# Performance work log

Measured on AMD Instinct MI355X. Metric: run time of the kernel, lower is better.

The kernel has to match this reference:

```python
import jax, jax.numpy as jnp
import numpy as np

HID = 128; L = 4; N = 100000; E = 1600000; B = 512; OUT = 1
NVOC = 101; EVOC = 21

def layer_norm(x, g, b, eps=1e-5):
    m = x.mean(-1, keepdims=True)
    v = ((x - m) ** 2).mean(-1, keepdims=True)
    return (x - m) * jax.lax.rsqrt(v + eps) * g + b

def setup_inputs() -> dict:
    key = jax.random.key(0)
    ks = jax.random.split(key, 20)
    s = 1.0 / np.sqrt(HID)
    return {
        "x_idx": jax.random.randint(ks[0], (N,), 0, NVOC),
        "edge_index": jax.random.randint(ks[1], (2, E), 0, N),
        "edge_attr": jax.random.randint(ks[2], (E, 3), 0, EVOC),
        "batch": jnp.sort(jax.random.randint(ks[3], (N,), 0, B)),
        "node_emb": jax.random.normal(ks[4], (NVOC, HID), jnp.float32) * 0.02,
        "e1": jax.random.normal(ks[5], (EVOC, HID), jnp.float32) * 0.02,
        "e2": jax.random.normal(ks[6], (EVOC, HID), jnp.float32) * 0.02,
        "e3": jax.random.normal(ks[7], (EVOC, HID), jnp.float32) * 0.02,
        "W1": jax.random.normal(ks[8], (L, HID, HID), jnp.float32) * s,
        "b1": jnp.zeros((L, HID), jnp.float32),
        "W2": jax.random.normal(ks[9], (L, HID, HID), jnp.float32) * s,
        "b2": jnp.zeros((L, HID), jnp.float32),
        "ln_g": jnp.ones((L, HID), jnp.float32),
        "ln_b": jnp.zeros((L, HID), jnp.float32),
        "pW1": jax.random.normal(ks[10], (HID, HID), jnp.float32) * s,
        "pb1": jnp.zeros((HID,), jnp.float32),
        "pW2": jax.random.normal(ks[11], (HID, HID), jnp.float32) * s,
        "pb2": jnp.zeros((HID,), jnp.float32),
        "pg": jnp.ones((HID,), jnp.float32),
        "pbn": jnp.zeros((HID,), jnp.float32),
        "oW": jax.random.normal(ks[12], (HID, OUT), jnp.float32) * s,
        "ob": jnp.zeros((OUT,), jnp.float32),
    }

def reference(x_idx, edge_index, edge_attr, batch, node_emb, e1, e2, e3,
              W1, b1, W2, b2, ln_g, ln_b, pW1, pb1, pW2, pb2, pg, pbn, oW, ob):
    # input embedding (inmlp) and bond embedding (edge_emb1+2+3)
    x = node_emb[x_idx]                                   # [N, H]
    bond = e1[edge_attr[:, 0]] + e2[edge_attr[:, 1]] + e3[edge_attr[:, 2]]  # [E, H]
    src, dst = edge_index[0], edge_index[1]
    # residual GINEConv stack: x = x + nn((1+eps)*x + sum_j relu(x_j + bond))
    for l in range(L):
        msg = jax.nn.relu(x[src] + bond)                  # gather + fuse
        agg = jax.ops.segment_sum(msg, dst, num_segments=N)  # scatter-add
        h = x + agg                                       # eps = 0
        h = jax.nn.relu(h @ W1[l] + b1[l])
        h = h @ W2[l] + b2[l]
        h = jax.nn.relu(layer_norm(h, ln_g[l], ln_b[l]))
        x = x + h
    # node-level mean pool per graph (node_pool='mean')
    sums = jax.ops.segment_sum(x, batch, num_segments=B)  # [B, H]
    cnt = jax.ops.segment_sum(jnp.ones((N, 1), x.dtype), batch, num_segments=B)
    g = sums / jnp.maximum(cnt, 1.0)
    h = jax.nn.relu(g @ pW1 + pb1)
    h = h @ pW2 + pb2
    h = jax.nn.relu(layer_norm(h, pg, pbn))
    return jax.nn.sigmoid(h @ oW + ob)                    # [B, 1]
```

## Files before the change

### kernel.cpp

```cpp
#include <hip/hip_runtime.h>

#define HID 128
#define NN  100000
#define EE  1600000
#define BB  512
#define LL  4

typedef __attribute__((ext_vector_type(8))) short bf16x8;
typedef __attribute__((ext_vector_type(4))) float f32x4;

__device__ __forceinline__ unsigned short f32_to_bf16(float f) {
    union { float f; unsigned u; } c; c.f = f;
    unsigned r = c.u + 0x7FFFu + ((c.u >> 16) & 1u);
    return (unsigned short)(r >> 16);
}
__device__ __forceinline__ float bf16_to_f32(unsigned short h) {
    union { unsigned u; float f; } c; c.u = ((unsigned)h) << 16; return c.f;
}

__global__ __launch_bounds__(256) void hist_kernel(
    const int* __restrict__ ei, int* __restrict__ R)
{
    int e = blockIdx.x * 256 + threadIdx.x;
    if (e >= EE) return;
    atomicAdd(&R[ei[EE + e] + 1], 1);
}

__global__ __launch_bounds__(256) void scan1_kernel(int* __restrict__ R,
                                                    int* __restrict__ aux, int n)
{
    __shared__ int sh[256];
    int base = blockIdx.x * 1024;
    int t = threadIdx.x;
    int v[4]; int s = 0;
#pragma unroll
    for (int i = 0; i < 4; ++i) {
        int idx = base + t * 4 + i;
        v[i] = (idx < n) ? R[idx] : 0;
        s += v[i];
    }
    sh[t] = s; __syncthreads();
#pragma unroll
    for (int off = 1; off < 256; off <<= 1) {
        int val = (t >= off) ? sh[t - off] : 0;
        __syncthreads();
        sh[t] += val;
        __syncthreads();
    }
    int run = (t == 0) ? 0 : sh[t - 1];
#pragma unroll
    for (int i = 0; i < 4; ++i) {
        int idx = base + t * 4 + i;
        run += v[i];
        if (idx < n) R[idx] = run;
    }
    if (t == 255) aux[blockIdx.x] = sh[255];
}

__global__ __launch_bounds__(128) void scan2_kernel(int* __restrict__ aux, int nb)
{
    __shared__ int sh[128];
    int t = threadIdx.x;
    sh[t] = (t < nb) ? aux[t] : 0;
    __syncthreads();
#pragma unroll
    for (int off = 1; off < 128; off <<= 1) {
        int val = (t >= off) ? sh[t - off] : 0;
        __syncthreads();
        sh[t] += val;
        __syncthreads();
    }
    if (t < nb) aux[t] = sh[t];
}

__global__ __launch_bounds__(256) void scan3_kernel(int* __restrict__ R,
                                                    const int* __restrict__ aux, int n)
{
    int b = blockIdx.x + 1;
    int add = aux[b - 1];
#pragma unroll
    for (int i = 0; i < 4; ++i) {
        int idx = b * 1024 + threadIdx.x * 4 + i;
        if (idx < n) R[idx] += add;
    }
}

__global__ __launch_bounds__(256) void fill_kernel(
    const int* __restrict__ ei, const int* __restrict__ ea,
    int* __restrict__ R, unsigned int* __restrict__ csr)
{
    int e = blockIdx.x * 256 + threadIdx.x;
    if (e >= EE) return;
    int pos = atomicAdd(&R[ei[EE + e]], 1);
    unsigned int rec = (unsigned int)ei[e]
                     | ((unsigned int)ea[e * 3 + 0] << 17)
                     | ((unsigned int)ea[e * 3 + 1] << 22)
                     | ((unsigned int)ea[e * 3 + 2] << 27);
    csr[pos] = rec;
}

__global__ __launch_bounds__(256) void embed_kernel(
    const int* __restrict__ x_idx, const float* __restrict__ node_emb,
    float* __restrict__ x)
{
    int t = blockIdx.x * 256 + threadIdx.x;
    int node = t >> 5, j = t & 31;
    if (node >= NN) return;
    ((float4*)x)[node * 32 + j] =
        ((const float4*)node_emb)[x_idx[node] * 32 + j];
}

__device__ __forceinline__ float4 edge_term(
    unsigned int rec, int l32, const float* __restrict__ x,
    const float* __restrict__ e1, const float* __restrict__ e2,
    const float* __restrict__ e3)
{
    int src = rec & 0x1FFFF;
    int i0 = (rec >> 17) & 31, i1 = (rec >> 22) & 31, i2 = (rec >> 27) & 31;
    float4 v  = ((const float4*)x )[src * 32 + l32];
    float4 w1 = ((const float4*)e1)[i0  * 32 + l32];
    float4 w2 = ((const float4*)e2)[i1  * 32 + l32];
    float4 w3 = ((const float4*)e3)[i2  * 32 + l32];
    float4 r;
    r.x = fmaxf(v.x + w1.x + w2.x + w3.x, 0.f);
    r.y = fmaxf(v.y + w1.y + w2.y + w3.y, 0.f);
    r.z = fmaxf(v.z + w1.z + w2.z + w3.z, 0.f);
    r.w = fmaxf(v.w + w1.w + w2.w + w3.w, 0.f);
    return r;
}

__global__ __launch_bounds__(256, 8) void gather_kernel(
    const float* __restrict__ x,
    const float* __restrict__ e1, const float* __restrict__ e2,
    const float* __restrict__ e3,
    const int* __restrict__ rowend, const unsigned int* __restrict__ csr,
    float* __restrict__ agg)
{
    int wid  = (blockIdx.x * 256 + threadIdx.x) >> 6;
    int lane = threadIdx.x & 63;
    int half = lane >> 5;
    int l32  = lane & 31;
    if (wid >= NN) return;
    int beg = (wid == 0) ? 0 : rowend[wid - 1];
    int end = rowend[wid];

    float4 a0 = make_float4(0.f, 0.f, 0.f, 0.f);
    float4 a1 = make_float4(0.f, 0.f, 0.f, 0.f);
    float4 a2 = make_float4(0.f, 0.f, 0.f, 0.f);
    float4 a3 = make_float4(0.f, 0.f, 0.f, 0.f);
    int p = beg + half;
    for (; p + 6 < end; p += 8) {
        unsigned int r0 = csr[p];
        unsigned int r1 = csr[p + 2];
        unsigned int r2 = csr[p + 4];
        unsigned int r3 = csr[p + 6];
        float4 t0 = edge_term(r0, l32, x, e1, e2, e3);
        float4 t1 = edge_term(r1, l32, x, e1, e2, e3);
        float4 t2 = edge_term(r2, l32, x, e1, e2, e3);
        float4 t3 = edge_term(r3, l32, x, e1, e2, e3);
        a0.x += t0.x; a0.y += t0.y; a0.z += t0.z; a0.w += t0.w;
        a1.x += t1.x; a1.y += t1.y; a1.z += t1.z; a1.w += t1.w;
        a2.x += t2.x; a2.y += t2.y; a2.z += t2.z; a2.w += t2.w;
        a3.x += t3.x; a3.y += t3.y; a3.z += t3.z; a3.w += t3.w;
    }
    for (; p < end; p += 2) {
        float4 t0 = edge_term(csr[p], l32, x, e1, e2, e3);
        a0.x += t0.x; a0.y += t0.y; a0.z += t0.z; a0.w += t0.w;
    }
    float4 acc;
    acc.x = (a0.x + a1.x) + (a2.x + a3.x);
    acc.y = (a0.y + a1.y) + (a2.y + a3.y);
    acc.z = (a0.z + a1.z) + (a2.z + a3.z);
    acc.w = (a0.w + a1.w) + (a2.w + a3.w);
    acc.x += __shfl_xor(acc.x, 32);
    acc.y += __shfl_xor(acc.y, 32);
    acc.z += __shfl_xor(acc.z, 32);
    acc.w += __shfl_xor(acc.w, 32);
    if (half == 0)
        ((float4*)agg)[wid * 32 + l32] = acc;
}

__global__ __launch_bounds__(256) void wprep_kernel(
    const float* __restrict__ W1, const float* __restrict__ W2,
    unsigned short* __restrict__ wf)
{
    int t = blockIdx.x * 256 + threadIdx.x;
    if (t >= LL * 2 * 16384) return;
    int layer = t >> 15;
    int rem = t & 32767;
    int mat = rem >> 14;
    int idx = rem & 16383;
    int k = idx >> 7, n = idx & 127;
    const float* W = (mat ? W2 : W1) + layer * 16384;
    float w = W[k * 128 + n];
    unsigned short hi = f32_to_bf16(w);
    unsigned short lo = f32_to_bf16(w - bf16_to_f32(hi));
    int nb = n >> 4, nl = n & 15, kstep = k >> 5, quad = (k >> 3) & 3, j = k & 7;
    int di = ((nb * 4 + kstep) * 64 + (quad * 16 + nl)) * 8 + j;
    unsigned short* base = wf + (size_t)((layer * 2 + mat) * 2) * 16384;
    base[di] = hi;
    base[16384 + di] = lo;
}

__global__ __launch_bounds__(256) void edge_kernel(
    const float* __restrict__ x, const int* __restrict__ ei,
    const int* __restrict__ ea, const float* __restrict__ e1,
    const float* __restrict__ e2, const float* __restrict__ e3,
    float* __restrict__ agg)
{
    int t = blockIdx.x * 256 + threadIdx.x;
    int e = t >> 5, j = t & 31;
    if (e >= EE) return;
    int src = ei[e];
    int dst = ei[EE + e];
    int a0 = ea[e * 3 + 0], a1 = ea[e * 3 + 1], a2 = ea[e * 3 + 2];
    float4 v  = ((const float4*)x )[src * 32 + j];
    float4 w1 = ((const float4*)e1)[a0  * 32 + j];
    float4 w2 = ((const float4*)e2)[a1  * 32 + j];
    float4 w3 = ((const float4*)e3)[a2  * 32 + j];
    float mx = fmaxf(v.x + w1.x + w2.x + w3.x, 0.f);
    float my = fmaxf(v.y + w1.y + w2.y + w3.y, 0.f);
    float mz = fmaxf(v.z + w1.z + w2.z + w3.z, 0.f);
    float mw = fmaxf(v.w + w1.w + w2.w + w3.w, 0.f);
    float* ag = agg + (size_t)dst * HID + j * 4;
    atomicAdd(ag + 0, mx);
    atomicAdd(ag + 1, my);
    atomicAdd(ag + 2, mz);
    atomicAdd(ag + 3, mw);
}

#define TPAD 136
#define UPAD 132

__global__ __launch_bounds__(256) void mlp_mfma_kernel(
    const float* __restrict__ xin, const float* __restrict__ agg,
    const unsigned short* __restrict__ wf,
    const float* __restrict__ b1, const float* __restrict__ b2,
    const float* __restrict__ gamma, const float* __restrict__ beta,
    float* __restrict__ x)
{
    __shared__ __align__(16) char smemA[17408];
    __shared__ __align__(16) unsigned short t_hi[32 * TPAD];
    __shared__ __align__(16) unsigned short t_lo[32 * TPAD];
    unsigned short* h_hi = (unsigned short*)smemA;
    unsigned short* h_lo = (unsigned short*)(smemA + 8704);
    float* u_s = (float*)smemA;

    int tid = threadIdx.x;
    int rbase = blockIdx.x * 32;

    for (int idx = tid; idx < 32 * 32; idx += 256) {
        int r = idx >> 5, c4 = idx & 31;
        float4 xv = ((const float4*)xin)[(rbase + r) * 32 + c4];
        float4 av = ((const float4*)agg)[(rbase + r) * 32 + c4];
        float h0 = xv.x + av.x, h1 = xv.y + av.y;
        float h2 = xv.z + av.z, h3 = xv.w + av.w;
        unsigned short i0 = f32_to_bf16(h0), i1 = f32_to_bf16(h1);
        unsigned short i2 = f32_to_bf16(h2), i3 = f32_to_bf16(h3);
        ushort4 vh = make_ushort4(i0, i1, i2, i3);
        ushort4 vl = make_ushort4(f32_to_bf16(h0 - bf16_to_f32(i0)),
                                  f32_to_bf16(h1 - bf16_to_f32(i1)),
                                  f32_to_bf16(h2 - bf16_to_f32(i2)),
                                  f32_to_bf16(h3 - bf16_to_f32(i3)));
        int o = r * TPAD + c4 * 4;
        *(ushort4*)&h_hi[o] = vh;
        *(ushort4*)&h_lo[o] = vl;
    }
    __syncthreads();

    int lane = tid & 63;
    int wave = tid >> 6;
    int rb   = wave & 1;
    int cbg  = (wave >> 1) * 4;
    int quad = lane >> 4, nl = lane & 15;
    int arow = rb * 16 + nl;

    const unsigned short* w1_hi = wf;
    const unsigned short* w1_lo = wf + 16384;
    const unsigned short* w2_hi = wf + 32768;
    const unsigned short* w2_lo = wf + 49152;

    {
        f32x4 acc[4] = {};
#pragma unroll
        for (int ks = 0; ks < 4; ++ks) {
            int koff = ks * 32 + quad * 8;
            bf16x8 a_hi = *(const bf16x8*)&h_hi[arow * TPAD + koff];
            bf16x8 a_lo = *(const bf16x8*)&h_lo[arow * TPAD + koff];
#pragma unroll
            for (int cb = 0; cb < 4; ++cb) {
                int off = (((cbg + cb) * 4 + ks) * 64 + lane) * 8;
                bf16x8 b_hi = *(const bf16x8*)&w1_hi[off];
                bf16x8 b_lo = *(const bf16x8*)&w1_lo[off];
                acc[cb] = __builtin_amdgcn_mfma_f32_16x16x32_bf16(a_hi, b_hi, acc[cb], 0, 0, 0);
                acc[cb] = __builtin_amdgcn_mfma_f32_16x16x32_bf16(a_lo, b_hi, acc[cb], 0, 0, 0);
                acc[cb] = __builtin_amdgcn_mfma_f32_16x16x32_bf16(a_hi, b_lo, acc[cb], 0, 0, 0);
            }
        }
#pragma unroll
        for (int cb = 0; cb < 4; ++cb) {
            int col = (cbg + cb) * 16 + nl;
            float bv = b1[col];
#pragma unroll
            for (int r = 0; r < 4; ++r) {
                int row = rb * 16 + quad * 4 + r;
                float v = fmaxf(acc[cb][r] + bv, 0.f);
                unsigned short hi = f32_to_bf16(v);
                t_hi[row * TPAD + col] = hi;
                t_lo[row * TPAD + col] = f32_to_bf16(v - bf16_to_f32(hi));
            }
        }
    }
    __syncthreads();

    {
        f32x4 acc[4] = {};
#pragma unroll
        for (int ks = 0; ks < 4; ++ks) {
            int koff = ks * 32 + quad * 8;
            bf16x8 a_hi = *(const bf16x8*)&t_hi[arow * TPAD + koff];
            bf16x8 a_lo = *(const bf16x8*)&t_lo[arow * TPAD + koff];
#pragma unroll
            for (int cb = 0; cb < 4; ++cb) {
                int off = (((cbg + cb) * 4 + ks) * 64 + lane) * 8;
                bf16x8 b_hi = *(const bf16x8*)&w2_hi[off];
                bf16x8 b_lo = *(const bf16x8*)&w2_lo[off];
                acc[cb] = __builtin_amdgcn_mfma_f32_16x16x32_bf16(a_hi, b_hi, acc[cb], 0, 0, 0);
                acc[cb] = __builtin_amdgcn_mfma_f32_16x16x32_bf16(a_lo, b_hi, acc[cb], 0, 0, 0);
                acc[cb] = __builtin_amdgcn_mfma_f32_16x16x32_bf16(a_hi, b_lo, acc[cb], 0, 0, 0);
            }
        }
#pragma unroll
        for (int cb = 0; cb < 4; ++cb) {
            int col = (cbg + cb) * 16 + nl;
            float bv = b2[col];
#pragma unroll
            for (int r = 0; r < 4; ++r) {
                int row = rb * 16 + quad * 4 + r;
                u_s[row * UPAD + col] = acc[cb][r] + bv;
            }
        }
    }
    __syncthreads();

    {
        int tc = tid & 31, tr = tid >> 5;
        float4 gv  = ((const float4*)gamma)[tc];
        float4 btv = ((const float4*)beta )[tc];
#pragma unroll
        for (int j = 0; j < 4; ++j) {
            float4 u4 = *(const float4*)&u_s[(tr * 4 + j) * UPAD + tc * 4];
            float s = u4.x + u4.y + u4.z + u4.w;
            float q = u4.x*u4.x + u4.y*u4.y + u4.z*u4.z + u4.w*u4.w;
#pragma unroll
            for (int off = 1; off < 32; off <<= 1) {
                s += __shfl_xor(s, off, 64);
                q += __shfl_xor(q, off, 64);
            }
            float m   = s * (1.f / 128.f);
            float var = q * (1.f / 128.f) - m * m;
            float rs  = rsqrtf(var + 1e-5f);
            int r = rbase + tr * 4 + j;
            float4 xo = ((float4*)x)[r * 32 + tc];
            float4 o;
            o.x = xo.x + fmaxf((u4.x - m) * rs * gv.x + btv.x, 0.f);
            o.y = xo.y + fmaxf((u4.y - m) * rs * gv.y + btv.y, 0.f);
            o.z = xo.z + fmaxf((u4.z - m) * rs * gv.z + btv.z, 0.f);
            o.w = xo.w + fmaxf((u4.w - m) * rs * gv.w + btv.w, 0.f);
            ((float4*)x)[r * 32 + tc] = o;
        }
    }
}

__global__ __launch_bounds__(256) void gemm_relu_kernel(
    const float* __restrict__ x, const float* __restrict__ agg,
    const float* __restrict__ W, const float* __restrict__ bias,
    float* __restrict__ t)
{
    __shared__ float h_s[32 * 129];
    int tid = threadIdx.x;
    int tc = tid & 31, tr = tid >> 5;
    int rbase = blockIdx.x * 32;
    for (int idx = tid; idx < 32 * 128; idx += 256) {
        int r = idx >> 7, k = idx & 127;
        int g = (rbase + r) * HID + k;
        h_s[r * 129 + k] = x[g] + agg[g];
    }
    __syncthreads();
    float acc[4][4] = {};
    const float4* W4 = (const float4*)W;
#pragma unroll 4
    for (int k = 0; k < 128; ++k) {
        float4 w = W4[k * 32 + tc];
#pragma unroll
        for (int j = 0; j < 4; ++j) {
            float hv = h_s[(tr * 4 + j) * 129 + k];
            acc[j][0] = fmaf(hv, w.x, acc[j][0]);
            acc[j][1] = fmaf(hv, w.y, acc[j][1]);
            acc[j][2] = fmaf(hv, w.z, acc[j][2]);
            acc[j][3] = fmaf(hv, w.w, acc[j][3]);
        }
    }
    float4 bv = ((const float4*)bias)[tc];
#pragma unroll
    for (int j = 0; j < 4; ++j) {
        int r = rbase + tr * 4 + j;
        float4 o;
        o.x = fmaxf(acc[j][0] + bv.x, 0.f);
        o.y = fmaxf(acc[j][1] + bv.y, 0.f);
        o.z = fmaxf(acc[j][2] + bv.z, 0.f);
        o.w = fmaxf(acc[j][3] + bv.w, 0.f);
        ((float4*)t)[r * 32 + tc] = o;
    }
}

__global__ __launch_bounds__(256) void gemm_ln_res_kernel(
    const float* __restrict__ t, const float* __restrict__ W,
    const float* __restrict__ bias, const float* __restrict__ gamma,
    const float* __restrict__ beta, float* __restrict__ x)
{
    __shared__ float h_s[32 * 129];
    int tid = threadIdx.x;
    int tc = tid & 31, tr = tid >> 5;
    int rbase = blockIdx.x * 32;
    for (int idx = tid; idx < 32 * 128; idx += 256) {
        int r = idx >> 7, k = idx & 127;
        h_s[r * 129 + k] = t[(rbase + r) * HID + k];
    }
    __syncthreads();
    float acc[4][4] = {};
    const float4* W4 = (const float4*)W;
#pragma unroll 4
    for (int k = 0; k < 128; ++k) {
        float4 w = W4[k * 32 + tc];
#pragma unroll
        for (int j = 0; j < 4; ++j) {
            float hv = h_s[(tr * 4 + j) * 129 + k];
            acc[j][0] = fmaf(hv, w.x, acc[j][0]);
            acc[j][1] = fmaf(hv, w.y, acc[j][1]);
            acc[j][2] = fmaf(hv, w.z, acc[j][2]);
            acc[j][3] = fmaf(hv, w.w, acc[j][3]);
        }
    }
    float4 bv  = ((const float4*)bias )[tc];
    float4 gv  = ((const float4*)gamma)[tc];
    float4 btv = ((const float4*)beta )[tc];
#pragma unroll
    for (int j = 0; j < 4; ++j) {
        acc[j][0] += bv.x; acc[j][1] += bv.y;
        acc[j][2] += bv.z; acc[j][3] += bv.w;
        float s = acc[j][0] + acc[j][1] + acc[j][2] + acc[j][3];
        float q = acc[j][0]*acc[j][0] + acc[j][1]*acc[j][1]
                + acc[j][2]*acc[j][2] + acc[j][3]*acc[j][3];
#pragma unroll
        for (int off = 1; off < 32; off <<= 1) {
            s += __shfl_xor(s, off, 64);
            q += __shfl_xor(q, off, 64);
        }
        float m   = s * (1.f / 128.f);
        float var = q * (1.f / 128.f) - m * m;
        float rs  = rsqrtf(var + 1e-5f);
        int r = rbase + tr * 4 + j;
        float4 xo = ((float4*)x)[r * 32 + tc];
        float4 o;
        o.x = xo.x + fmaxf((acc[j][0] - m) * rs * gv.x + btv.x, 0.f);
        o.y = xo.y + fmaxf((acc[j][1] - m) * rs * gv.y + btv.y, 0.f);
        o.z = xo.z + fmaxf((acc[j][2] - m) * rs * gv.z + btv.z, 0.f);
        o.w = xo.w + fmaxf((acc[j][3] - m) * rs * gv.w + btv.w, 0.f);
        ((float4*)x)[r * 32 + tc] = o;
    }
}

#define PCHUNK 32
__global__ __launch_bounds__(256) void pool_kernel(
    const float* __restrict__ x, const int* __restrict__ batch,
    float* __restrict__ sums, int* __restrict__ cnt)
{
    int wave = (blockIdx.x * 256 + threadIdx.x) >> 6;
    int lane = threadIdx.x & 63;
    int n0 = wave * PCHUNK;
    if (n0 >= NN) return;
    int n1 = n0 + PCHUNK; if (n1 > NN) n1 = NN;

    float2 acc = make_float2(0.f, 0.f);
    int cur = batch[n0];
    int run = 0;
    for (int n = n0; n < n1; ++n) {
        int b = batch[n];
        if (b != cur) {
            float* sp = sums + cur * HID + lane * 2;
            atomicAdd(sp + 0, acc.x);
            atomicAdd(sp + 1, acc.y);
            if (lane == 0) atomicAdd(&cnt[cur], run);
            acc = make_float2(0.f, 0.f);
            run = 0; cur = b;
        }
        float2 v = ((const float2*)x)[(size_t)n * 64 + lane];
        acc.x += v.x; acc.y += v.y; ++run;
    }
    float* sp = sums + cur * HID + lane * 2;
    atomicAdd(sp + 0, acc.x);
    atomicAdd(sp + 1, acc.y);
    if (lane == 0) atomicAdd(&cnt[cur], run);
}

__global__ __launch_bounds__(128) void head_kernel(
    const float* __restrict__ sums, const int* __restrict__ cnt,
    const float* __restrict__ pW1, const float* __restrict__ pb1,
    const float* __restrict__ pW2, const float* __restrict__ pb2,
    const float* __restrict__ pg, const float* __restrict__ pbn,
    const float* __restrict__ oW, const float* __restrict__ ob,
    float* __restrict__ out)
{
    __shared__ float s0[128], s1[128], red[4];
    int b = blockIdx.x, c = threadIdx.x;

    float cn = fmaxf((float)cnt[b], 1.f);
    s0[c] = sums[b * HID + c] / cn;
    __syncthreads();

    float a = pb1[c];
#pragma unroll 4
    for (int k = 0; k < HID; ++k) a = fmaf(s0[k], pW1[k * HID + c], a);
    a = fmaxf(a, 0.f);
    s1[c] = a;
    __syncthreads();

    float u = pb2[c];
#pragma unroll 4
    for (int k = 0; k < HID; ++k) u = fmaf(s1[k], pW2[k * HID + c], u);

    float s = u, q = u * u;
#pragma unroll
    for (int off = 1; off < 64; off <<= 1) {
        s += __shfl_xor(s, off, 64);
        q += __shfl_xor(q, off, 64);
    }
    if ((c & 63) == 0) { red[(c >> 6) * 2] = s; red[(c >> 6) * 2 + 1] = q; }
    __syncthreads();
    float S = red[0] + red[2], Q = red[1] + red[3];
    float m = S * (1.f / 128.f);
    float var = Q * (1.f / 128.f) - m * m;
    float rs = rsqrtf(var + 1e-5f);
    float v = fmaxf((u - m) * rs * pg[c] + pbn[c], 0.f);

    float p = v * oW[c];
#pragma unroll
    for (int off = 1; off < 64; off <<= 1) p += __shfl_xor(p, off, 64);
    __syncthreads();
    if ((c & 63) == 0) red[c >> 6] = p;
    __syncthreads();
    if (c == 0) {
        float tot = red[0] + red[1] + ob[0];
        out[b] = 1.f / (1.f + expf(-tot));
    }
}

extern "C" void kernel_launch(void* const* d_in, const int* in_sizes, int n_in,
                              void* d_out, int out_size, void* d_ws, size_t ws_size,
                              hipStream_t stream)
{
    const int*   x_idx    = (const int*)d_in[0];
    const int*   ei       = (const int*)d_in[1];
    const int*   ea       = (const int*)d_in[2];
    const int*   batch    = (const int*)d_in[3];
    const float* node_emb = (const float*)d_in[4];
    const float* e1       = (const float*)d_in[5];
    const float* e2       = (const float*)d_in[6];
    const float* e3       = (const float*)d_in[7];
    const float* W1       = (const float*)d_in[8];
    const float* b1       = (const float*)d_in[9];
    const float* W2       = (const float*)d_in[10];
    const float* b2       = (const float*)d_in[11];
    const float* lg       = (const float*)d_in[12];
    const float* lb       = (const float*)d_in[13];
    const float* pW1      = (const float*)d_in[14];
    const float* pb1      = (const float*)d_in[15];
    const float* pW2      = (const float*)d_in[16];
    const float* pb2      = (const float*)d_in[17];
    const float* pg       = (const float*)d_in[18];
    const float* pbn      = (const float*)d_in[19];
    const float* oW       = (const float*)d_in[20];
    const float* ob       = (const float*)d_in[21];
    float* out = (float*)d_out;

    char* base = (char*)d_ws;
    size_t Sx = (size_t)NN * HID * sizeof(float);
    float* x    = (float*)(base);
    float* agg  = (float*)(base + Sx);
    float* sums = (float*)(base + 2 * Sx);
    int*   cnt  = (int*)  (base + 2 * Sx + BB * HID * 4);
    int*   R    = (int*)  (base + 2 * Sx + BB * HID * 4 + 2048);
    unsigned int* csr = (unsigned int*)((char*)R + 400016);
    int*   aux  = (int*)  ((char*)csr + (size_t)EE * 4);
    unsigned short* wf = (unsigned short*)((char*)aux + 512);
    size_t need = ((char*)wf + (size_t)LL * 2 * 2 * 16384 * 2) - base;

    bool fast = (ws_size >= need);

    embed_kernel<<<(NN * 32 + 255) / 256, 256, 0, stream>>>(x_idx, node_emb, x);

    if (fast) {
        const int n = NN + 1, NB = (n + 1023) / 1024;
        hipMemsetAsync(R, 0, (size_t)n * sizeof(int), stream);
        hist_kernel <<<(EE + 255) / 256, 256, 0, stream>>>(ei, R);
        scan1_kernel<<<NB, 256, 0, stream>>>(R, aux, n);
        scan2_kernel<<<1, 128, 0, stream>>>(aux, NB);
        scan3_kernel<<<NB - 1, 256, 0, stream>>>(R, aux, n);
        fill_kernel <<<(EE + 255) / 256, 256, 0, stream>>>(ei, ea, R, csr);
        wprep_kernel<<<(LL * 2 * 16384 + 255) / 256, 256, 0, stream>>>(W1, W2, wf);
    }

    for (int l = 0; l < LL; ++l) {
        if (fast) {
            gather_kernel<<<(NN * 64 + 255) / 256, 256, 0, stream>>>(
                x, e1, e2, e3, R, csr, agg);
            mlp_mfma_kernel<<<NN / 32, 256, 0, stream>>>(
                x, agg, wf + (size_t)l * 65536,
                b1 + l * HID, b2 + l * HID,
                lg + l * HID, lb + l * HID, x);
        } else {
            hipMemsetAsync(agg, 0, Sx, stream);
            edge_kernel<<<(EE * 32 + 255) / 256, 256, 0, stream>>>(
                x, ei, ea, e1, e2, e3, agg);
            gemm_relu_kernel<<<NN / 32, 256, 0, stream>>>(
                x, agg, W1 + l * HID * HID, b1 + l * HID, agg);
            gemm_ln_res_kernel<<<NN / 32, 256, 0, stream>>>(
                agg, W2 + l * HID * HID, b2 + l * HID,
                lg + l * HID, lb + l * HID, x);
        }
    }

    hipMemsetAsync(sums, 0,
                   (size_t)BB * HID * sizeof(float) + BB * sizeof(int), stream);
    {
        int waves = (NN + PCHUNK - 1) / PCHUNK;
        int blocks = (waves + 3) / 4;
        pool_kernel<<<blocks, 256, 0, stream>>>(x, batch, sums, cnt);
    }
    head_kernel<<<BB, 128, 0, stream>>>(
        sums, cnt, pW1, pb1, pW2, pb2, pg, pbn, oW, ob, out);
}
```

Measured before the change: 1.326 ms.

## Fuse CSR gather with MLP into one per-layer kernel using ping-pong x buffers

Merges the per-node CSR gather and the two-GEMM MLP with LayerNorm into a single kernel per layer. Each block handles 16 nodes, and each wave gathers 4 nodes straight into bf16 hi/lo shared tiles. The agg buffer is replaced by double-buffered x to avoid read/write hazards across blocks. This removes the write and re-read of the 51 MB agg tensor and one launch per layer. In exchange, MFMA tiles shrink to 16 rows, so weight reuse per block is lower, and gather latency is no longer overlapped with GEMM work inside the block.

```diff
diff --git a/kernel.cpp b/kernel.cpp
--- a/kernel.cpp
+++ b/kernel.cpp
@@ -5,6 +5,7 @@
 #define EE  1600000
 #define BB  512
 #define LL  4
+#define FROWS 16
 
 typedef __attribute__((ext_vector_type(8))) short bf16x8;
 typedef __attribute__((ext_vector_type(4))) float f32x4;
@@ -108,76 +109,6 @@
     if (node >= NN) return;
     ((float4*)x)[node * 32 + j] =
         ((const float4*)node_emb)[x_idx[node] * 32 + j];
-}
-
-__device__ __forceinline__ float4 edge_term(
-    unsigned int rec, int l32, const float* __restrict__ x,
-    const float* __restrict__ e1, const float* __restrict__ e2,
-    const float* __restrict__ e3)
-{
-    int src = rec & 0x1FFFF;
-    int i0 = (rec >> 17) & 31, i1 = (rec >> 22) & 31, i2 = (rec >> 27) & 31;
-    float4 v  = ((const float4*)x )[src * 32 + l32];
-    float4 w1 = ((const float4*)e1)[i0  * 32 + l32];
-    float4 w2 = ((const float4*)e2)[i1  * 32 + l32];
-    float4 w3 = ((const float4*)e3)[i2  * 32 + l32];
-    float4 r;
-    r.x = fmaxf(v.x + w1.x + w2.x + w3.x, 0.f);
-    r.y = fmaxf(v.y + w1.y + w2.y + w3.y, 0.f);
-    r.z = fmaxf(v.z + w1.z + w2.z + w3.z, 0.f);
-    r.w = fmaxf(v.w + w1.w + w2.w + w3.w, 0.f);
-    return r;
-}
-
-__global__ __launch_bounds__(256, 8) void gather_kernel(
-    const float* __restrict__ x,
-    const float* __restrict__ e1, const float* __restrict__ e2,
-    const float* __restrict__ e3,
-    const int* __restrict__ rowend, const unsigned int* __restrict__ csr,
-    float* __restrict__ agg)
-{
-    int wid  = (blockIdx.x * 256 + threadIdx.x) >> 6;
-    int lane = threadIdx.x & 63;
-    int half = lane >> 5;
-    int l32  = lane & 31;
-    if (wid >= NN) return;
-    int beg = (wid == 0) ? 0 : rowend[wid - 1];
-    int end = rowend[wid];
-
-    float4 a0 = make_float4(0.f, 0.f, 0.f, 0.f);
-    float4 a1 = make_float4(0.f, 0.f, 0.f, 0.f);
-    float4 a2 = make_float4(0.f, 0.f, 0.f, 0.f);
-    float4 a3 = make_float4(0.f, 0.f, 0.f, 0.f);
-    int p = beg + half;
-    for (; p + 6 < end; p += 8) {
-        unsigned int r0 = csr[p];
-        unsigned int r1 = csr[p + 2];
-        unsigned int r2 = csr[p + 4];
-        unsigned int r3 = csr[p + 6];
-        float4 t0 = edge_term(r0, l32, x, e1, e2, e3);
-        float4 t1 = edge_term(r1, l32, x, e1, e2, e3);
-        float4 t2 = edge_term(r2, l32, x, e1, e2, e3);
-        float4 t3 = edge_term(r3, l32, x, e1, e2, e3);
-        a0.x += t0.x; a0.y += t0.y; a0.z += t0.z; a0.w += t0.w;
-        a1.x += t1.x; a1.y += t1.y; a1.z += t1.z; a1.w += t1.w;
-        a2.x += t2.x; a2.y += t2.y; a2.z += t2.z; a2.w += t2.w;
-        a3.x += t3.x; a3.y += t3.y; a3.z += t3.z; a3.w += t3.w;
-    }
-    for (; p < end; p += 2) {
-        float4 t0 = edge_term(csr[p], l32, x, e1, e2, e3);
-        a0.x += t0.x; a0.y += t0.y; a0.z += t0.z; a0.w += t0.w;
-    }
-    float4 acc;
-    acc.x = (a0.x + a1.x) + (a2.x + a3.x);
-    acc.y = (a0.y + a1.y) + (a2.y + a3.y);
-    acc.z = (a0.z + a1.z) + (a2.z + a3.z);
-    acc.w = (a0.w + a1.w) + (a2.w + a3.w);
-    acc.x += __shfl_xor(acc.x, 32);
-    acc.y += __shfl_xor(acc.y, 32);
-    acc.z += __shfl_xor(acc.z, 32);
-    acc.w += __shfl_xor(acc.w, 32);
-    if (half == 0)
-        ((float4*)agg)[wid * 32 + l32] = acc;
 }
 
 __global__ __launch_bounds__(256) void wprep_kernel(
@@ -200,6 +131,206 @@
     unsigned short* base = wf + (size_t)((layer * 2 + mat) * 2) * 16384;
     base[di] = hi;
     base[16384 + di] = lo;
+}
+
+__device__ __forceinline__ float4 edge_term(
+    unsigned int rec, int l32, const float* __restrict__ x,
+    const float* __restrict__ e1, const float* __restrict__ e2,
+    const float* __restrict__ e3)
+{
+    int src = rec & 0x1FFFF;
+    int i0 = (rec >> 17) & 31, i1 = (rec >> 22) & 31, i2 = (rec >> 27) & 31;
+    float4 v  = ((const float4*)x )[src * 32 + l32];
+    float4 w1 = ((const float4*)e1)[i0  * 32 + l32];
+    float4 w2 = ((const float4*)e2)[i1  * 32 + l32];
+    float4 w3 = ((const float4*)e3)[i2  * 32 + l32];
+    float4 r;
+    r.x = fmaxf(v.x + w1.x + w2.x + w3.x, 0.f);
+    r.y = fmaxf(v.y + w1.y + w2.y + w3.y, 0.f);
+    r.z = fmaxf(v.z + w1.z + w2.z + w3.z, 0.f);
+    r.w = fmaxf(v.w + w1.w + w2.w + w3.w, 0.f);
+    return r;
+}
+
+#define TPAD 136
+#define UPAD 132
+
+__global__ __launch_bounds__(256) void layer_fused_kernel(
+    const float* __restrict__ xin,
+    const float* __restrict__ e1, const float* __restrict__ e2,
+    const float* __restrict__ e3,
+    const int* __restrict__ rowend, const unsigned int* __restrict__ csr,
+    const unsigned short* __restrict__ wf,
+    const float* __restrict__ b1, const float* __restrict__ b2,
+    const float* __restrict__ gamma, const float* __restrict__ beta,
+    float* __restrict__ xout)
+{
+    __shared__ __align__(16) char smemA[8704];
+    __shared__ __align__(16) unsigned short t_hi[FROWS * TPAD];
+    __shared__ __align__(16) unsigned short t_lo[FROWS * TPAD];
+    unsigned short* h_hi = (unsigned short*)smemA;
+    unsigned short* h_lo = (unsigned short*)(smemA + 4352);
+    float* u_s = (float*)smemA;
+
+    int tid = threadIdx.x;
+    int rbase = blockIdx.x * FROWS;
+    int w = tid >> 6;
+    int lane = tid & 63;
+    int half = lane >> 5;
+    int l32  = lane & 31;
+
+    for (int ln = w * 4; ln < w * 4 + 4; ++ln) {
+        int node = rbase + ln;
+        int beg = (node == 0) ? 0 : rowend[node - 1];
+        int end = rowend[node];
+
+        float4 a0 = make_float4(0.f, 0.f, 0.f, 0.f);
+        float4 a1 = make_float4(0.f, 0.f, 0.f, 0.f);
+        float4 a2 = make_float4(0.f, 0.f, 0.f, 0.f);
+        float4 a3 = make_float4(0.f, 0.f, 0.f, 0.f);
+        int p = beg + half;
+        for (; p + 6 < end; p += 8) {
+            unsigned int r0 = csr[p];
+            unsigned int r1 = csr[p + 2];
+            unsigned int r2 = csr[p + 4];
+            unsigned int r3 = csr[p + 6];
+            float4 t0 = edge_term(r0, l32, xin, e1, e2, e3);
+            float4 t1 = edge_term(r1, l32, xin, e1, e2, e3);
+            float4 t2 = edge_term(r2, l32, xin, e1, e2, e3);
+            float4 t3 = edge_term(r3, l32, xin, e1, e2, e3);
+            a0.x += t0.x; a0.y += t0.y; a0.z += t0.z; a0.w += t0.w;
+            a1.x += t1.x; a1.y += t1.y; a1.z += t1.z; a1.w += t1.w;
+            a2.x += t2.x; a2.y += t2.y; a2.z += t2.z; a2.w += t2.w;
+            a3.x += t3.x; a3.y += t3.y; a3.z += t3.z; a3.w += t3.w;
+        }
+        for (; p < end; p += 2) {
+            float4 t0 = edge_term(csr[p], l32, xin, e1, e2, e3);
+            a0.x += t0.x; a0.y += t0.y; a0.z += t0.z; a0.w += t0.w;
+        }
+        float4 acc;
+        acc.x = (a0.x + a1.x) + (a2.x + a3.x);
+        acc.y = (a0.y + a1.y) + (a2.y + a3.y);
+        acc.z = (a0.z + a1.z) + (a2.z + a3.z);
+        acc.w = (a0.w + a1.w) + (a2.w + a3.w);
+        acc.x += __shfl_xor(acc.x, 32);
+        acc.y += __shfl_xor(acc.y, 32);
+        acc.z += __shfl_xor(acc.z, 32);
+        acc.w += __shfl_xor(acc.w, 32);
+        if (half == 0) {
+            float4 xv = ((const float4*)xin)[node * 32 + l32];
+            float h0 = xv.x + acc.x, h1 = xv.y + acc.y;
+            float h2 = xv.z + acc.z, h3 = xv.w + acc.w;
+            unsigned short i0 = f32_to_bf16(h0), i1 = f32_to_bf16(h1);
+            unsigned short i2 = f32_to_bf16(h2), i3 = f32_to_bf16(h3);
+            int o = ln * TPAD + l32 * 4;
+            *(ushort4*)&h_hi[o] = make_ushort4(i0, i1, i2, i3);
+            *(ushort4*)&h_lo[o] =
+                make_ushort4(f32_to_bf16(h0 - bf16_to_f32(i0)),
+                             f32_to_bf16(h1 - bf16_to_f32(i1)),
+                             f32_to_bf16(h2 - bf16_to_f32(i2)),
+                             f32_to_bf16(h3 - bf16_to_f32(i3)));
+        }
+    }
+    __syncthreads();
+
+    int quad = lane >> 4, nl = lane & 15;
+    int cbg = w * 2;
+    const unsigned short* w1_hi = wf;
+    const unsigned short* w1_lo = wf + 16384;
+    const unsigned short* w2_hi = wf + 32768;
+    const unsigned short* w2_lo = wf + 49152;
+
+    {
+        f32x4 acc[2] = {};
+#pragma unroll
+        for (int ks = 0; ks < 4; ++ks) {
+            int koff = ks * 32 + quad * 8;
+            bf16x8 a_hi = *(const bf16x8*)&h_hi[nl * TPAD + koff];
+            bf16x8 a_lo = *(const bf16x8*)&h_lo[nl * TPAD + koff];
+#pragma unroll
+            for (int cb = 0; cb < 2; ++cb) {
+                int off = (((cbg + cb) * 4 + ks) * 64 + lane) * 8;
+                bf16x8 b_hi = *(const bf16x8*)&w1_hi[off];
+                bf16x8 b_lo = *(const bf16x8*)&w1_lo[off];
+                acc[cb] = __builtin_amdgcn_mfma_f32_16x16x32_bf16(a_hi, b_hi, acc[cb], 0, 0, 0);
+                acc[cb] = __builtin_amdgcn_mfma_f32_16x16x32_bf16(a_lo, b_hi, acc[cb], 0, 0, 0);
+                acc[cb] = __builtin_amdgcn_mfma_f32_16x16x32_bf16(a_hi, b_lo, acc[cb], 0, 0, 0);
+            }
+        }
+#pragma unroll
+        for (int cb = 0; cb < 2; ++cb) {
+            int col = (cbg + cb) * 16 + nl;
+            float bv = b1[col];
+#pragma unroll
+            for (int r = 0; r < 4; ++r) {
+                int row = quad * 4 + r;
+                float v = fmaxf(acc[cb][r] + bv, 0.f);
+                unsigned short hi = f32_to_bf16(v);
+                t_hi[row * TPAD + col] = hi;
+                t_lo[row * TPAD + col] = f32_to_bf16(v - bf16_to_f32(hi));
+            }
+        }
+    }
+    __syncthreads();
+
+    {
+        f32x4 acc[2] = {};
+#pragma unroll
+        for (int ks = 0; ks < 4; ++ks) {
+            int koff = ks * 32 + quad * 8;
+            bf16x8 a_hi = *(const bf16x8*)&t_hi[nl * TPAD + koff];
+            bf16x8 a_lo = *(const bf16x8*)&t_lo[nl * TPAD + koff];
+#pragma unroll
+            for (int cb = 0; cb < 2; ++cb) {
+                int off = (((cbg + cb) * 4 + ks) * 64 + lane) * 8;
+                bf16x8 b_hi = *(const bf16x8*)&w2_hi[off];
+                bf16x8 b_lo = *(const bf16x8*)&w2_lo[off];
+                acc[cb] = __builtin_amdgcn_mfma_f32_16x16x32_bf16(a_hi, b_hi, acc[cb], 0, 0, 0);
+                acc[cb] = __builtin_amdgcn_mfma_f32_16x16x32_bf16(a_lo, b_hi, acc[cb], 0, 0, 0);
+                acc[cb] = __builtin_amdgcn_mfma_f32_16x16x32_bf16(a_hi, b_lo, acc[cb], 0, 0, 0);
+            }
+        }
+#pragma unroll
+        for (int cb = 0; cb < 2; ++cb) {
+            int col = (cbg + cb) * 16 + nl;
+            float bv = b2[col];
+#pragma unroll
+            for (int r = 0; r < 4; ++r) {
+                int row = quad * 4 + r;
+                u_s[row * UPAD + col] = acc[cb][r] + bv;
+            }
+        }
+    }
+    __syncthreads();
+
+    {
+        int tc = tid & 31, tr = tid >> 5;
+        float4 gv  = ((const float4*)gamma)[tc];
+        float4 btv = ((const float4*)beta )[tc];
+#pragma unroll
+        for (int j = 0; j < 2; ++j) {
+            int row = tr * 2 + j;
+            float4 u4 = *(const float4*)&u_s[row * UPAD + tc * 4];
+            float s = u4.x + u4.y + u4.z + u4.w;
+            float q = u4.x*u4.x + u4.y*u4.y + u4.z*u4.z + u4.w*u4.w;
+#pragma unroll
+            for (int off = 1; off < 32; off <<= 1) {
+                s += __shfl_xor(s, off, 64);
+                q += __shfl_xor(q, off, 64);
+            }
+            float m   = s * (1.f / 128.f);
+            float var = q * (1.f / 128.f) - m * m;
+            float rs  = rsqrtf(var + 1e-5f);
+            int g = rbase + row;
+            float4 xo = ((const float4*)xin)[g * 32 + tc];
+            float4 o;
+            o.x = xo.x + fmaxf((u4.x - m) * rs * gv.x + btv.x, 0.f);
+            o.y = xo.y + fmaxf((u4.y - m) * rs * gv.y + btv.y, 0.f);
+            o.z = xo.z + fmaxf((u4.z - m) * rs * gv.z + btv.z, 0.f);
+            o.w = xo.w + fmaxf((u4.w - m) * rs * gv.w + btv.w, 0.f);
+            ((float4*)xout)[g * 32 + tc] = o;
+        }
+    }
 }
 
 __global__ __launch_bounds__(256) void edge_kernel(
@@ -227,149 +358,6 @@
     atomicAdd(ag + 1, my);
     atomicAdd(ag + 2, mz);
     atomicAdd(ag + 3, mw);
-}
-
-#define TPAD 136
-#define UPAD 132
-
-__global__ __launch_bounds__(256) void mlp_mfma_kernel(
-    const float* __restrict__ xin, const float* __restrict__ agg,
-    const unsigned short* __restrict__ wf,
-    const float* __restrict__ b1, const float* __restrict__ b2,
-    const float* __restrict__ gamma, const float* __restrict__ beta,
-    float* __restrict__ x)
-{
-    __shared__ __align__(16) char smemA[17408];
-    __shared__ __align__(16) unsigned short t_hi[32 * TPAD];
-    __shared__ __align__(16) unsigned short t_lo[32 * TPAD];
-    unsigned short* h_hi = (unsigned short*)smemA;
-    unsigned short* h_lo = (unsigned short*)(smemA + 8704);
-    float* u_s = (float*)smemA;
-
-    int tid = threadIdx.x;
-    int rbase = blockIdx.x * 32;
-
-    for (int idx = tid; idx < 32 * 32; idx += 256) {
-        int r = idx >> 5, c4 = idx & 31;
-        float4 xv = ((const float4*)xin)[(rbase + r) * 32 + c4];
-        float4 av = ((const float4*)agg)[(rbase + r) * 32 + c4];
-        float h0 = xv.x + av.x, h1 = xv.y + av.y;
-        float h2 = xv.z + av.z, h3 = xv.w + av.w;
-        unsigned short i0 = f32_to_bf16(h0), i1 = f32_to_bf16(h1);
-        unsigned short i2 = f32_to_bf16(h2), i3 = f32_to_bf16(h3);
-        ushort4 vh = make_ushort4(i0, i1, i2, i3);
-        ushort4 vl = make_ushort4(f32_to_bf16(h0 - bf16_to_f32(i0)),
-                                  f32_to_bf16(h1 - bf16_to_f32(i1)),
-                                  f32_to_bf16(h2 - bf16_to_f32(i2)),
-                                  f32_to_bf16(h3 - bf16_to_f32(i3)));
-        int o = r * TPAD + c4 * 4;
-        *(ushort4*)&h_hi[o] = vh;
-        *(ushort4*)&h_lo[o] = vl;
-    }
-    __syncthreads();
-
-    int lane = tid & 63;
-    int wave = tid >> 6;
-    int rb   = wave & 1;
-    int cbg  = (wave >> 1) * 4;
-    int quad = lane >> 4, nl = lane & 15;
-    int arow = rb * 16 + nl;
-
-    const unsigned short* w1_hi = wf;
-    const unsigned short* w1_lo = wf + 16384;
-    const unsigned short* w2_hi = wf + 32768;
-    const unsigned short* w2_lo = wf + 49152;
-
-    {
-        f32x4 acc[4] = {};
-#pragma unroll
-        for (int ks = 0; ks < 4; ++ks) {
-            int koff = ks * 32 + quad * 8;
-            bf16x8 a_hi = *(const bf16x8*)&h_hi[arow * TPAD + koff];
-            bf16x8 a_lo = *(const bf16x8*)&h_lo[arow * TPAD + koff];
-#pragma unroll
-            for (int cb = 0; cb < 4; ++cb) {
-                int off = (((cbg + cb) * 4 + ks) * 64 + lane) * 8;
-                bf16x8 b_hi = *(const bf16x8*)&w1_hi[off];
-                bf16x8 b_lo = *(const bf16x8*)&w1_lo[off];
-                acc[cb] = __builtin_amdgcn_mfma_f32_16x16x32_bf16(a_hi, b_hi, acc[cb], 0, 0, 0);
-                acc[cb] = __builtin_amdgcn_mfma_f32_16x16x32_bf16(a_lo, b_hi, acc[cb], 0, 0, 0);
-                acc[cb] = __builtin_amdgcn_mfma_f32_16x16x32_bf16(a_hi, b_lo, acc[cb], 0, 0, 0);
-            }
-        }
-#pragma unroll
-        for (int cb = 0; cb < 4; ++cb) {
-            int col = (cbg + cb) * 16 + nl;
-            float bv = b1[col];
-#pragma unroll
-            for (int r = 0; r < 4; ++r) {
-                int row = rb * 16 + quad * 4 + r;
-                float v = fmaxf(acc[cb][r] + bv, 0.f);
-                unsigned short hi = f32_to_bf16(v);
-                t_hi[row * TPAD + col] = hi;
-                t_lo[row * TPAD + col] = f32_to_bf16(v - bf16_to_f32(hi));
-            }
-        }
-    }
-    __syncthreads();
-
-    {
-        f32x4 acc[4] = {};
-#pragma unroll
-        for (int ks = 0; ks < 4; ++ks) {
-            int koff = ks * 32 + quad * 8;
-            bf16x8 a_hi = *(const bf16x8*)&t_hi[arow * TPAD + koff];
-            bf16x8 a_lo = *(const bf16x8*)&t_lo[arow * TPAD + koff];
-#pragma unroll
-            for (int cb = 0; cb < 4; ++cb) {
-                int off = (((cbg + cb) * 4 + ks) * 64 + lane) * 8;
-                bf16x8 b_hi = *(const bf16x8*)&w2_hi[off];
-                bf16x8 b_lo = *(const bf16x8*)&w2_lo[off];
-                acc[cb] = __builtin_amdgcn_mfma_f32_16x16x32_bf16(a_hi, b_hi, acc[cb], 0, 0, 0);
-                acc[cb] = __builtin_amdgcn_mfma_f32_16x16x32_bf16(a_lo, b_hi, acc[cb], 0, 0, 0);
-                acc[cb] = __builtin_amdgcn_mfma_f32_16x16x32_bf16(a_hi, b_lo, acc[cb], 0, 0, 0);
-            }
-        }
-#pragma unroll
-        for (int cb = 0; cb < 4; ++cb) {
-            int col = (cbg + cb) * 16 + nl;
-            float bv = b2[col];
-#pragma unroll
-            for (int r = 0; r < 4; ++r) {
-                int row = rb * 16 + quad * 4 + r;
-                u_s[row * UPAD + col] = acc[cb][r] + bv;
-            }
-        }
-    }
-    __syncthreads();
-
-    {
-        int tc = tid & 31, tr = tid >> 5;
-        float4 gv  = ((const float4*)gamma)[tc];
-        float4 btv = ((const float4*)beta )[tc];
-#pragma unroll
-        for (int j = 0; j < 4; ++j) {
-            float4 u4 = *(const float4*)&u_s[(tr * 4 + j) * UPAD + tc * 4];
-            float s = u4.x + u4.y + u4.z + u4.w;
-            float q = u4.x*u4.x + u4.y*u4.y + u4.z*u4.z + u4.w*u4.w;
-#pragma unroll
-            for (int off = 1; off < 32; off <<= 1) {
-                s += __shfl_xor(s, off, 64);
-                q += __shfl_xor(q, off, 64);
-            }
-            float m   = s * (1.f / 128.f);
-            float var = q * (1.f / 128.f) - m * m;
-            float rs  = rsqrtf(var + 1e-5f);
-            int r = rbase + tr * 4 + j;
-            float4 xo = ((float4*)x)[r * 32 + tc];
-            float4 o;
-            o.x = xo.x + fmaxf((u4.x - m) * rs * gv.x + btv.x, 0.f);
-            o.y = xo.y + fmaxf((u4.y - m) * rs * gv.y + btv.y, 0.f);
-            o.z = xo.z + fmaxf((u4.z - m) * rs * gv.z + btv.z, 0.f);
-            o.w = xo.w + fmaxf((u4.w - m) * rs * gv.w + btv.w, 0.f);
-            ((float4*)x)[r * 32 + tc] = o;
-        }
-    }
 }
 
 __global__ __launch_bounds__(256) void gemm_relu_kernel(
@@ -586,8 +574,8 @@
 
     char* base = (char*)d_ws;
     size_t Sx = (size_t)NN * HID * sizeof(float);
-    float* x    = (float*)(base);
-    float* agg  = (float*)(base + Sx);
+    float* x0   = (float*)(base);
+    float* x1   = (float*)(base + Sx);
     float* sums = (float*)(base + 2 * Sx);
     int*   cnt  = (int*)  (base + 2 * Sx + BB * HID * 4);
     int*   R    = (int*)  (base + 2 * Sx + BB * HID * 4 + 2048);
@@ -598,7 +586,7 @@
 
     bool fast = (ws_size >= need);
 
-    embed_kernel<<<(NN * 32 + 255) / 256, 256, 0, stream>>>(x_idx, node_emb, x);
+    embed_kernel<<<(NN * 32 + 255) / 256, 256, 0, stream>>>(x_idx, node_emb, x0);
 
     if (fast) {
         const int n = NN + 1, NB = (n + 1023) / 1024;
@@ -609,17 +597,19 @@
         scan3_kernel<<<NB - 1, 256, 0, stream>>>(R, aux, n);
         fill_kernel <<<(EE + 255) / 256, 256, 0, stream>>>(ei, ea, R, csr);
         wprep_kernel<<<(LL * 2 * 16384 + 255) / 256, 256, 0, stream>>>(W1, W2, wf);
-    }
-
-    for (int l = 0; l < LL; ++l) {
-        if (fast) {
-            gather_kernel<<<(NN * 64 + 255) / 256, 256, 0, stream>>>(
-                x, e1, e2, e3, R, csr, agg);
-            mlp_mfma_kernel<<<NN / 32, 256, 0, stream>>>(
-                x, agg, wf + (size_t)l * 65536,
+
+        for (int l = 0; l < LL; ++l) {
+            const float* xin = (l & 1) ? x1 : x0;
+            float*       xo  = (l & 1) ? x0 : x1;
+            layer_fused_kernel<<<NN / FROWS, 256, 0, stream>>>(
+                xin, e1, e2, e3, R, csr, wf + (size_t)l * 65536,
                 b1 + l * HID, b2 + l * HID,
-                lg + l * HID, lb + l * HID, x);
-        } else {
+                lg + l * HID, lb + l * HID, xo);
+        }
+    } else {
+        float* x   = x0;
+        float* agg = x1;
+        for (int l = 0; l < LL; ++l) {
             hipMemsetAsync(agg, 0, Sx, stream);
             edge_kernel<<<(EE * 32 + 255) / 256, 256, 0, stream>>>(
                 x, ei, ea, e1, e2, e3, agg);
@@ -636,7 +626,7 @@
     {
         int waves = (NN + PCHUNK - 1) / PCHUNK;
         int blocks = (waves + 3) / 4;
-        pool_kernel<<<blocks, 256, 0, stream>>>(x, batch, sums, cnt);
+        pool_kernel<<<blocks, 256, 0, stream>>>(x0, batch, sums, cnt);
     }
     head_kernel<<<BB, 128, 0, stream>>>(
         sums, cnt, pW1, pb1, pW2, pb2, pg, pbn, oW, ob, out);
```

Measured after the change: 1.085 ms. 1.22x faster.
